# Performance work log

Hardware: AMD Instinct MI355X
Metric: run time of the kernel (lower is better)

## Reference

```python
import jax, jax.numpy as jnp
import numpy as np

DIM = 64
RANK = 8
K = 16
SPLIT = [1, DIM, DIM * RANK, DIM]
OUT_DIM = sum(SPLIT) * K  # 10256
B = 8192


def setup_inputs() -> dict:
    key = jax.random.key(0)
    k1, k2 = jax.random.split(key)
    pred = jax.random.normal(k1, (B, OUT_DIM), dtype=jnp.float32)
    label = jax.random.normal(k2, (B, DIM), dtype=jnp.float32)
    return {"pred": pred, "label": label}


def _format(pred):
    out = pred.reshape(-1, K, sum(SPLIT))
    o1 = 1
    o2 = o1 + DIM
    o3 = o2 + DIM * RANK
    pis = out[..., 0]                                   # [B, K] categorical logits
    mus = out[..., o1:o2]                               # [B, K, D]
    cov_factors = out[..., o2:o3].reshape(-1, K, DIM, RANK)  # [B, K, D, R]
    cov_diags = jnp.exp(out[..., o3:])                  # [B, K, D], positive
    return pis, mus, cov_factors, cov_diags


def _gmm_nll(pred, label):
    pis, mus, W, d = _format(pred)
    diff = label[:, None, :] - mus                      # [B, K, D]
    dinv = 1.0 / d
    # Woodbury capacitance: C = I_r + W^T D^{-1} W   -> [B, K, R, R]
    cap = jnp.einsum('bkdr,bkd,bkds->bkrs', W, dinv, W)
    cap = cap + jnp.eye(RANK, dtype=pred.dtype)
    L = jnp.linalg.cholesky(cap)                        # [B, K, R, R]
    # Mahalanobis via Woodbury: d^T D^-1 d - ||L^-1 W^T D^-1 d||^2
    b = jnp.einsum('bkdr,bkd->bkr', W, diff * dinv)     # W^T D^{-1} diff
    y = jax.scipy.linalg.solve_triangular(L, b[..., None], lower=True)[..., 0]
    mahal = jnp.sum(diff * diff * dinv, axis=-1) - jnp.sum(y * y, axis=-1)
    # log|Sigma| = 2*sum(log diag L) + sum(log d)
    logdet = 2.0 * jnp.sum(jnp.log(jnp.diagonal(L, axis1=-2, axis2=-1)), axis=-1) \
             + jnp.sum(jnp.log(d), axis=-1)
    log2pi = jnp.asarray(np.log(2.0 * np.pi), dtype=pred.dtype)
    comp_lp = -0.5 * (DIM * log2pi + logdet + mahal)    # [B, K]
    log_mix = jax.nn.log_softmax(pis, axis=-1)          # [B, K]
    return -jax.scipy.special.logsumexp(log_mix + comp_lp, axis=-1)  # [B]


def reference(pred, label):
    return _gmm_nll(pred, label)
```

## Files before the change

### kernel.cpp

```cpp
#include <hip/hip_runtime.h>

#define NDIM 64
#define NRANK 8
#define NK 16
#define CSTRIDE 641
#define ROWSTRIDE (CSTRIDE * NK)


template <int CTRL>
__device__ __forceinline__ float dpp_mov(float x) {
  int t = __builtin_amdgcn_update_dpp(0, __builtin_bit_cast(int, x), CTRL,
                                      0xF, 0xF, true);
  return __builtin_bit_cast(float, t);
}

__device__ __forceinline__ void red16(float& x) {
  x += dpp_mov<0xB1>(x);
  x += dpp_mov<0x4E>(x);
  x += dpp_mov<0x141>(x);
  x += dpp_mov<0x140>(x);
}

__device__ __forceinline__ void gld_lds16(const float* g, float* l) {
  __builtin_amdgcn_global_load_lds(
      (const __attribute__((address_space(1))) void*)g,
      (__attribute__((address_space(3))) void*)l, 16, 0, 0);
}


__global__ __launch_bounds__(256) void gmm_nll_kernel(
    const float* __restrict__ pred, const float* __restrict__ label,
    float* __restrict__ out, int nb) {
  __shared__ float lds[10528];
  const int tid = threadIdx.x;
  const int w = tid >> 6;
  const int lane = tid & 63;
  const int kk = lane >> 4;
  const int de = lane & 15;
  const int b = blockIdx.x;

  const float* rowg = pred + (size_t)b * ROWSTRIDE;
  const float* lbl = label + (size_t)b * NDIM;

  float lb_[4];
  lb_[0] = lbl[de];
  lb_[1] = lbl[de + 16];
  lb_[2] = lbl[de + 32];
  lb_[3] = lbl[de + 48];
  asm volatile("" ::: "memory");

  const bool last = (b == nb - 1);
#pragma unroll
  for (int t = 0; t <= 10; ++t) {
    const int j = 10 * w + t;
    const float* src = rowg + j * 256 + lane * 4;
    float* dst = &lds[j * 256];
    if (j < 40) {
      gld_lds16(src, dst);
    } else {
      if (!last) {
        gld_lds16(src, dst);
      } else if (lane < 4) {
        gld_lds16(src, dst);
      }
    }
  }
  asm volatile("s_waitcnt vmcnt(0)" ::: "memory");

  const int k = 4 * w + kk;
  const int C0 = CSTRIDE * k;

  float capL[NRANK][NRANK];
  float bv[NRANK];
#pragma unroll
  for (int r = 0; r < NRANK; ++r) {
    bv[r] = 0.f;
#pragma unroll
    for (int s = 0; s <= r; ++s) capL[r][s] = 0.f;
  }
  float mahal1 = 0.f, ldsum = 0.f;

#pragma unroll
  for (int i = 0; i < 4; ++i) {
    const int d = de + 16 * i;
    float mu = lds[C0 + 1 + d];
    float ldv = lds[C0 + 577 + d];
    float sd = __expf(-0.5f * ldv);
    float diff = lb_[i] - mu;
    float u = diff * sd;
    mahal1 = fmaf(u, u, mahal1);
    ldsum += ldv;

    float v[NRANK];
#pragma unroll
    for (int r = 0; r < NRANK; ++r) v[r] = lds[C0 + 65 + 8 * d + r] * sd;
#pragma unroll
    for (int r = 0; r < NRANK; ++r) {
      bv[r] = fmaf(v[r], u, bv[r]);
#pragma unroll
      for (int s = 0; s <= r; ++s)
        capL[r][s] = fmaf(v[r], v[s], capL[r][s]);
    }
  }

  red16(mahal1);
  red16(ldsum);
#pragma unroll
  for (int r = 0; r < NRANK; ++r) {
    red16(bv[r]);
#pragma unroll
    for (int s = 0; s <= r; ++s) red16(capL[r][s]);
  }

#pragma unroll
  for (int r = 0; r < NRANK; ++r) capL[r][r] += 1.0f;

  float invd[NRANK];
  float prodinv = 1.0f;
#pragma unroll
  for (int j = 0; j < NRANK; ++j) {
    float s = capL[j][j];
#pragma unroll
    for (int p = 0; p < j; ++p) s = fmaf(-capL[j][p], capL[j][p], s);
    float inv = __frsqrt_rn(s);
    invd[j] = inv;
    prodinv *= inv;
#pragma unroll
    for (int i2 = j + 1; i2 < NRANK; ++i2) {
      float t = capL[i2][j];
#pragma unroll
      for (int p = 0; p < j; ++p) t = fmaf(-capL[i2][p], capL[j][p], t);
      capL[i2][j] = t * inv;
    }
  }
  float logdetL = -__logf(prodinv);

  float y[NRANK];
  float ysq = 0.f;
#pragma unroll
  for (int i2 = 0; i2 < NRANK; ++i2) {
    float t = bv[i2];
#pragma unroll
    for (int j = 0; j < i2; ++j) t = fmaf(-capL[i2][j], y[j], t);
    y[i2] = t * invd[i2];
    ysq = fmaf(y[i2], y[i2], ysq);
  }

  float mahal = mahal1 - ysq;
  float logdet = 2.0f * logdetL + ldsum;
  const float c_dim_log2pi = 117.62413225019810f;
  float comp_lp = -0.5f * (c_dim_log2pi + logdet + mahal);

  float pi = lds[C0];

  if (de == 0) {
    lds[10496 + k] = pi;
    lds[10496 + 16 + k] = pi + comp_lp;
  }
  __syncthreads();

  if (tid < 16) {
    float p = lds[10496 + tid];
    float t2 = lds[10496 + 16 + tid];

    float m1 = p;
    m1 = fmaxf(m1, dpp_mov<0xB1>(m1));
    m1 = fmaxf(m1, dpp_mov<0x4E>(m1));
    m1 = fmaxf(m1, dpp_mov<0x141>(m1));
    m1 = fmaxf(m1, dpp_mov<0x140>(m1));
    float e1 = __expf(p - m1);
    red16(e1);

    float m2 = t2;
    m2 = fmaxf(m2, dpp_mov<0xB1>(m2));
    m2 = fmaxf(m2, dpp_mov<0x4E>(m2));
    m2 = fmaxf(m2, dpp_mov<0x141>(m2));
    m2 = fmaxf(m2, dpp_mov<0x140>(m2));
    float e2 = __expf(t2 - m2);
    red16(e2);

    if (tid == 0)
      out[b] = (m1 + __logf(e1)) - (m2 + __logf(e2));
  }
}

extern "C" void kernel_launch(void* const* d_in, const int* in_sizes, int n_in,
                              void* d_out, int out_size, void* d_ws,
                              size_t ws_size, hipStream_t stream) {
  const float* pred = (const float*)d_in[0];
  const float* label = (const float*)d_in[1];
  float* out = (float*)d_out;
  const int nb = out_size;
  gmm_nll_kernel<<<dim3(nb), dim3(256), 0, stream>>>(pred, label, out, nb);
}
```

Baseline: 64.73 us.

## Make GMM NLL kernel persistent and prefetch the next row into LDS

The kernel now launches a fixed grid of 768 blocks that loop over batch rows with stride 768, instead of one block per row. Each wave owns the quarter of the row that holds its four components. After it finishes reading that quarter from LDS, it issues the async global-to-LDS loads for its quarter of the next row, and loads the next labels into registers. This overlaps the next row's memory traffic with the reductions, Cholesky and logsumexp of the current row, and removes per-block launch and ramp-up costs. The trade-off is fewer blocks to hide latency and an extra barrier per iteration, on a kernel that is largely bound by memory bandwidth.

```diff
diff --git a/kernel.cpp b/kernel.cpp
--- a/kernel.cpp
+++ b/kernel.cpp
@@ -5,6 +5,8 @@
 #define NK 16
 #define CSTRIDE 641
 #define ROWSTRIDE (CSTRIDE * NK)
+#define QBYTES (ROWSTRIDE)
+#define GRID_BLOCKS 768
 
 
 template <int CTRL>
@@ -21,7 +23,7 @@
   x += dpp_mov<0x140>(x);
 }
 
-__device__ __forceinline__ void gld_lds16(const float* g, float* l) {
+__device__ __forceinline__ void gld_lds16(const void* g, void* l) {
   __builtin_amdgcn_global_load_lds(
       (const __attribute__((address_space(1))) void*)g,
       (__attribute__((address_space(3))) void*)l, 16, 0, 0);
@@ -31,156 +33,166 @@
 __global__ __launch_bounds__(256) void gmm_nll_kernel(
     const float* __restrict__ pred, const float* __restrict__ label,
     float* __restrict__ out, int nb) {
-  __shared__ float lds[10528];
+  __shared__ float lds[ROWSTRIDE + 32];
   const int tid = threadIdx.x;
   const int w = tid >> 6;
   const int lane = tid & 63;
   const int kk = lane >> 4;
   const int de = lane & 15;
-  const int b = blockIdx.x;
-
-  const float* rowg = pred + (size_t)b * ROWSTRIDE;
-  const float* lbl = label + (size_t)b * NDIM;
-
-  float lb_[4];
-  lb_[0] = lbl[de];
-  lb_[1] = lbl[de + 16];
-  lb_[2] = lbl[de + 32];
-  lb_[3] = lbl[de + 48];
-  asm volatile("" ::: "memory");
-
-  const bool last = (b == nb - 1);
-#pragma unroll
-  for (int t = 0; t <= 10; ++t) {
-    const int j = 10 * w + t;
-    const float* src = rowg + j * 256 + lane * 4;
-    float* dst = &lds[j * 256];
-    if (j < 40) {
-      gld_lds16(src, dst);
-    } else {
-      if (!last) {
-        gld_lds16(src, dst);
-      } else if (lane < 4) {
-        gld_lds16(src, dst);
-      }
-    }
-  }
-  asm volatile("s_waitcnt vmcnt(0)" ::: "memory");
 
   const int k = 4 * w + kk;
   const int C0 = CSTRIDE * k;
 
-  float capL[NRANK][NRANK];
-  float bv[NRANK];
-#pragma unroll
-  for (int r = 0; r < NRANK; ++r) {
-    bv[r] = 0.f;
-#pragma unroll
-    for (int s = 0; s <= r; ++s) capL[r][s] = 0.f;
+  char* qdst = (char*)lds + (size_t)QBYTES * w;
+
+  int b = blockIdx.x;
+
+  {
+    const char* qsrc =
+        (const char*)(pred + (size_t)b * ROWSTRIDE) + QBYTES * w + 16 * lane;
+#pragma unroll
+    for (int t = 0; t < 10; ++t) gld_lds16(qsrc + 1024 * t, qdst + 1024 * t);
+    if (lane == 0) gld_lds16(qsrc + 10240, qdst + 10240);
   }
-  float mahal1 = 0.f, ldsum = 0.f;
-
-#pragma unroll
-  for (int i = 0; i < 4; ++i) {
-    const int d = de + 16 * i;
-    float mu = lds[C0 + 1 + d];
-    float ldv = lds[C0 + 577 + d];
-    float sd = __expf(-0.5f * ldv);
-    float diff = lb_[i] - mu;
-    float u = diff * sd;
-    mahal1 = fmaf(u, u, mahal1);
-    ldsum += ldv;
-
-    float v[NRANK];
-#pragma unroll
-    for (int r = 0; r < NRANK; ++r) v[r] = lds[C0 + 65 + 8 * d + r] * sd;
+  float lb_[4];
+  {
+    const float* lbl = label + (size_t)b * NDIM + de;
+    lb_[0] = lbl[0]; lb_[1] = lbl[16]; lb_[2] = lbl[32]; lb_[3] = lbl[48];
+  }
+
+  for (;;) {
+    asm volatile("s_waitcnt vmcnt(0)" ::: "memory");
+
+    float capL[NRANK][NRANK];
+    float bv[NRANK];
 #pragma unroll
     for (int r = 0; r < NRANK; ++r) {
-      bv[r] = fmaf(v[r], u, bv[r]);
-#pragma unroll
-      for (int s = 0; s <= r; ++s)
-        capL[r][s] = fmaf(v[r], v[s], capL[r][s]);
-    }
-  }
-
-  red16(mahal1);
-  red16(ldsum);
-#pragma unroll
-  for (int r = 0; r < NRANK; ++r) {
-    red16(bv[r]);
-#pragma unroll
-    for (int s = 0; s <= r; ++s) red16(capL[r][s]);
-  }
-
-#pragma unroll
-  for (int r = 0; r < NRANK; ++r) capL[r][r] += 1.0f;
-
-  float invd[NRANK];
-  float prodinv = 1.0f;
-#pragma unroll
-  for (int j = 0; j < NRANK; ++j) {
-    float s = capL[j][j];
-#pragma unroll
-    for (int p = 0; p < j; ++p) s = fmaf(-capL[j][p], capL[j][p], s);
-    float inv = __frsqrt_rn(s);
-    invd[j] = inv;
-    prodinv *= inv;
-#pragma unroll
-    for (int i2 = j + 1; i2 < NRANK; ++i2) {
-      float t = capL[i2][j];
-#pragma unroll
-      for (int p = 0; p < j; ++p) t = fmaf(-capL[i2][p], capL[j][p], t);
-      capL[i2][j] = t * inv;
-    }
-  }
-  float logdetL = -__logf(prodinv);
-
-  float y[NRANK];
-  float ysq = 0.f;
-#pragma unroll
-  for (int i2 = 0; i2 < NRANK; ++i2) {
-    float t = bv[i2];
-#pragma unroll
-    for (int j = 0; j < i2; ++j) t = fmaf(-capL[i2][j], y[j], t);
-    y[i2] = t * invd[i2];
-    ysq = fmaf(y[i2], y[i2], ysq);
-  }
-
-  float mahal = mahal1 - ysq;
-  float logdet = 2.0f * logdetL + ldsum;
-  const float c_dim_log2pi = 117.62413225019810f;
-  float comp_lp = -0.5f * (c_dim_log2pi + logdet + mahal);
-
-  float pi = lds[C0];
-
-  if (de == 0) {
-    lds[10496 + k] = pi;
-    lds[10496 + 16 + k] = pi + comp_lp;
-  }
-  __syncthreads();
-
-  if (tid < 16) {
-    float p = lds[10496 + tid];
-    float t2 = lds[10496 + 16 + tid];
-
-    float m1 = p;
-    m1 = fmaxf(m1, dpp_mov<0xB1>(m1));
-    m1 = fmaxf(m1, dpp_mov<0x4E>(m1));
-    m1 = fmaxf(m1, dpp_mov<0x141>(m1));
-    m1 = fmaxf(m1, dpp_mov<0x140>(m1));
-    float e1 = __expf(p - m1);
-    red16(e1);
-
-    float m2 = t2;
-    m2 = fmaxf(m2, dpp_mov<0xB1>(m2));
-    m2 = fmaxf(m2, dpp_mov<0x4E>(m2));
-    m2 = fmaxf(m2, dpp_mov<0x141>(m2));
-    m2 = fmaxf(m2, dpp_mov<0x140>(m2));
-    float e2 = __expf(t2 - m2);
-    red16(e2);
-
-    if (tid == 0)
-      out[b] = (m1 + __logf(e1)) - (m2 + __logf(e2));
+      bv[r] = 0.f;
+#pragma unroll
+      for (int s = 0; s <= r; ++s) capL[r][s] = 0.f;
+    }
+    float mahal1 = 0.f, ldsum = 0.f;
+
+#pragma unroll
+    for (int i = 0; i < 4; ++i) {
+      const int d = de + 16 * i;
+      float mu = lds[C0 + 1 + d];
+      float ldv = lds[C0 + 577 + d];
+      float sd = __expf(-0.5f * ldv);
+      float diff = lb_[i] - mu;
+      float u = diff * sd;
+      mahal1 = fmaf(u, u, mahal1);
+      ldsum += ldv;
+
+      float v[NRANK];
+#pragma unroll
+      for (int r = 0; r < NRANK; ++r) v[r] = lds[C0 + 65 + 8 * d + r] * sd;
+#pragma unroll
+      for (int r = 0; r < NRANK; ++r) {
+        bv[r] = fmaf(v[r], u, bv[r]);
+#pragma unroll
+        for (int s = 0; s <= r; ++s)
+          capL[r][s] = fmaf(v[r], v[s], capL[r][s]);
+      }
+    }
+    float pi = lds[C0];
+
+    asm volatile("s_waitcnt lgkmcnt(0)" ::: "memory");
+
+    const int nextb = b + GRID_BLOCKS;
+    const bool more = nextb < nb;
+    float lbn[4];
+    if (more) {
+      const char* qsrc = (const char*)(pred + (size_t)nextb * ROWSTRIDE) +
+                         QBYTES * w + 16 * lane;
+#pragma unroll
+      for (int t = 0; t < 10; ++t) gld_lds16(qsrc + 1024 * t, qdst + 1024 * t);
+      if (lane == 0) gld_lds16(qsrc + 10240, qdst + 10240);
+      const float* lbl = label + (size_t)nextb * NDIM + de;
+      lbn[0] = lbl[0]; lbn[1] = lbl[16]; lbn[2] = lbl[32]; lbn[3] = lbl[48];
+    }
+
+    red16(mahal1);
+    red16(ldsum);
+#pragma unroll
+    for (int r = 0; r < NRANK; ++r) {
+      red16(bv[r]);
+#pragma unroll
+      for (int s = 0; s <= r; ++s) red16(capL[r][s]);
+    }
+
+#pragma unroll
+    for (int r = 0; r < NRANK; ++r) capL[r][r] += 1.0f;
+
+    float invd[NRANK];
+    float prodinv = 1.0f;
+#pragma unroll
+    for (int j = 0; j < NRANK; ++j) {
+      float s = capL[j][j];
+#pragma unroll
+      for (int p = 0; p < j; ++p) s = fmaf(-capL[j][p], capL[j][p], s);
+      float inv = __frsqrt_rn(s);
+      invd[j] = inv;
+      prodinv *= inv;
+#pragma unroll
+      for (int i2 = j + 1; i2 < NRANK; ++i2) {
+        float t = capL[i2][j];
+#pragma unroll
+        for (int p = 0; p < j; ++p) t = fmaf(-capL[i2][p], capL[j][p], t);
+        capL[i2][j] = t * inv;
+      }
+    }
+    float logdetL = -__logf(prodinv);
+
+    float y[NRANK];
+    float ysq = 0.f;
+#pragma unroll
+    for (int i2 = 0; i2 < NRANK; ++i2) {
+      float t = bv[i2];
+#pragma unroll
+      for (int j = 0; j < i2; ++j) t = fmaf(-capL[i2][j], y[j], t);
+      y[i2] = t * invd[i2];
+      ysq = fmaf(y[i2], y[i2], ysq);
+    }
+
+    float mahal = mahal1 - ysq;
+    float logdet = 2.0f * logdetL + ldsum;
+    const float c_dim_log2pi = 117.62413225019810f;
+    float comp_lp = -0.5f * (c_dim_log2pi + logdet + mahal);
+
+    if (de == 0) {
+      lds[ROWSTRIDE + k] = pi;
+      lds[ROWSTRIDE + 16 + k] = pi + comp_lp;
+    }
+    __syncthreads();
+
+    if (tid < 16) {
+      float p = lds[ROWSTRIDE + tid];
+      float t2 = lds[ROWSTRIDE + 16 + tid];
+
+      float m1 = p;
+      m1 = fmaxf(m1, dpp_mov<0xB1>(m1));
+      m1 = fmaxf(m1, dpp_mov<0x4E>(m1));
+      m1 = fmaxf(m1, dpp_mov<0x141>(m1));
+      m1 = fmaxf(m1, dpp_mov<0x140>(m1));
+      float e1 = __expf(p - m1);
+      red16(e1);
+
+      float m2 = t2;
+      m2 = fmaxf(m2, dpp_mov<0xB1>(m2));
+      m2 = fmaxf(m2, dpp_mov<0x4E>(m2));
+      m2 = fmaxf(m2, dpp_mov<0x141>(m2));
+      m2 = fmaxf(m2, dpp_mov<0x140>(m2));
+      float e2 = __expf(t2 - m2);
+      red16(e2);
+
+      if (tid == 0) out[b] = (m1 + __logf(e1)) - (m2 + __logf(e2));
+    }
+    __syncthreads();
+
+    if (!more) break;
+    b = nextb;
+    lb_[0] = lbn[0]; lb_[1] = lbn[1]; lb_[2] = lbn[2]; lb_[3] = lbn[3];
   }
 }
 
@@ -191,5 +203,6 @@
   const float* label = (const float*)d_in[1];
   float* out = (float*)d_out;
   const int nb = out_size;
-  gmm_nll_kernel<<<dim3(nb), dim3(256), 0, stream>>>(pred, label, out, nb);
-}
+  gmm_nll_kernel<<<dim3(GRID_BLOCKS), dim3(256), 0, stream>>>(pred, label, out,
+                                                              nb);
+}
```

Result: slower. 67.12 us (+3.7%).
